# Kernel optimization log

Hardware: AMD Instinct MI355X
Metric: run time of the kernel (lower is better)

## Reference

```python
import jax, jax.numpy as jnp
from jax import lax
import numpy as np

B, C_IN, H, W = 8, 64, 128, 128
C_OUT, K = 64, 3
STRIDE, PAD, DIL = 1, 1, 1
KK = K * K
H_OUT = (H + 2 * PAD - DIL * (K - 1) - 1) // STRIDE + 1
W_OUT = (W + 2 * PAD - DIL * (K - 1) - 1) // STRIDE + 1


def setup_inputs() -> dict:
    key = jax.random.key(0)
    k1, k2, k3, k4 = jax.random.split(key, 4)
    x = jax.random.normal(k1, (B, C_IN, H, W), jnp.float32)
    # offset-predicting conv params (zero-init in the module; use small random
    # values so the deformable sampling path is actually exercised)
    offset_w = jax.random.normal(k2, (2 * KK, C_IN, K, K), jnp.float32) * 0.01
    offset_b = jax.random.normal(k3, (2 * KK,), jnp.float32) * 0.01
    weight = jax.random.normal(k4, (C_OUT, C_IN, K, K), jnp.float32) * (1.0 / np.sqrt(C_IN * KK))
    return {"x": x, "offset_w": offset_w, "offset_b": offset_b, "weight": weight}


def reference(x, offset_w, offset_b, weight):
    # 1) predict offsets: [B, 2*K*K, Hout, Wout], layout (dy, dx) per kernel tap
    offset = lax.conv_general_dilated(
        x, offset_w, (STRIDE, STRIDE), ((PAD, PAD), (PAD, PAD)),
        rhs_dilation=(DIL, DIL), dimension_numbers=("NCHW", "OIHW", "NCHW"))
    offset = offset + offset_b[None, :, None, None]
    off = offset.reshape(B, KK, 2, H_OUT, W_OUT)
    dy = off[:, :, 0].transpose(0, 2, 3, 1)  # [B, Hout, Wout, KK]
    dx = off[:, :, 1].transpose(0, 2, 3, 1)

    # 2) absolute sampling positions p = base_grid + learned offset
    ki, kj = jnp.meshgrid(jnp.arange(K), jnp.arange(K), indexing="ij")
    ki = ki.reshape(-1)
    kj = kj.reshape(-1)
    base_y = (jnp.arange(H_OUT) * STRIDE - PAD)[:, None, None] + ki[None, None, :] * DIL
    base_x = (jnp.arange(W_OUT) * STRIDE - PAD)[None, :, None] + kj[None, None, :] * DIL
    py = base_y[None].astype(x.dtype) + dy  # [B, Hout, Wout, KK]
    px = base_x[None].astype(x.dtype) + dx

    y0 = jnp.floor(py)
    x0 = jnp.floor(px)
    wy1 = py - y0
    wy0 = 1.0 - wy1
    wx1 = px - x0
    wx0 = 1.0 - wx1
    y0i = y0.astype(jnp.int32)
    x0i = x0.astype(jnp.int32)
    y1i = y0i + 1
    x1i = x0i + 1

    L = H_OUT * W_OUT * KK
    f = lambda a: a.reshape(B, L)

    def gather(xb, yi, xi):
        # xb: [C, H, W]; yi, xi: [L] int; zero outside the image
        valid = ((yi >= 0) & (yi < H) & (xi >= 0) & (xi < W)).astype(xb.dtype)
        idx = jnp.clip(yi, 0, H - 1) * W + jnp.clip(xi, 0, W - 1)
        return jnp.take(xb.reshape(C_IN, H * W), idx, axis=1) * valid[None]

    def per_batch(xb, y0i, y1i, x0i, x1i, wy0, wy1, wx0, wx1):
        return (gather(xb, y0i, x0i) * (wy0 * wx0)[None]
                + gather(xb, y0i, x1i) * (wy0 * wx1)[None]
                + gather(xb, y1i, x0i) * (wy1 * wx0)[None]
                + gather(xb, y1i, x1i) * (wy1 * wx1)[None])  # [C, L]

    sampled = jax.vmap(per_batch)(x, f(y0i), f(y1i), f(x0i), f(x1i),
                                  f(wy0), f(wy1), f(wx0), f(wx1))  # [B, C, L]
    sampled = sampled.reshape(B, C_IN, H_OUT, W_OUT, KK)

    # 3) im2col-style contraction against the conv weight (bias=None)
    out = jnp.einsum("bchwk,ock->bohw", sampled, weight.reshape(C_OUT, C_IN, KK))
    return out
```

## Files before the change

### kernel.cpp

```cpp
#include <hip/hip_runtime.h>

#define BATCH 8
#define CIN   64
#define COUT  64
#define HDIM  128
#define WDIM  128
#define HW    (HDIM * WDIM)
#define KK    9

typedef __attribute__((ext_vector_type(8)))  short  short8v;
typedef __attribute__((ext_vector_type(8)))  __bf16 bf16x8;
typedef __attribute__((ext_vector_type(16))) float  f32x16;
typedef float __attribute__((ext_vector_type(2), aligned(4))) float2u;

__device__ __forceinline__ short f2bf(float f) {
    unsigned u = __float_as_uint(f);
    return (short)((u + 0x7fffu + ((u >> 16) & 1u)) >> 16);
}
__device__ __forceinline__ float bf2f(short s) {
    return __uint_as_float(((unsigned)(unsigned short)s) << 16);
}
__device__ __forceinline__ f32x16 mfma_bf16(short8v a, short8v b, f32x16 c) {
    return __builtin_amdgcn_mfma_f32_32x32x16_bf16(
        __builtin_bit_cast(bf16x8, a), __builtin_bit_cast(bf16x8, b), c, 0, 0, 0);
}

__global__ __launch_bounds__(64) void wprep_kernel(
    const float* __restrict__ w, short* __restrict__ Wf)
{
    const int l   = threadIdx.x;
    const int blk = blockIdx.x;
    const int mt  = blk & 1;
    const int s   = blk >> 1;
    const int cg  = s / 9;
    const int t   = s - cg * 9;
    const int oc  = mt * 32 + (l & 31);
    const int cb  = cg * 16 + (l >> 5) * 8;
    short* p0 = Wf + ((size_t)blk * 2 + 0) * 512 + l * 8;
    short* p1 = Wf + ((size_t)blk * 2 + 1) * 512 + l * 8;
#pragma unroll
    for (int e = 0; e < 8; ++e) {
        float v = w[((size_t)oc * CIN + (cb + e)) * KK + t];
        short h = f2bf(v);
        p0[e] = h;
        p1[e] = f2bf(v - bf2f(h));
    }
}

__global__ __launch_bounds__(256) void offset_conv_kernel(
    const float* __restrict__ x,
    const float* __restrict__ ow,
    const float* __restrict__ ob,
    float* __restrict__ py,
    float* __restrict__ px)
{
    __shared__ float Xs[2][4][132];

    const int tid = threadIdx.x;
    const int lin = blockIdx.x;
    const int b   = lin & 7;
    const int par = (lin >> 3) & 1;
    const int pg  = lin >> 4;
    const int h0  = pg * 2;
    const int hh  = tid >> 7;
    const int w   = tid & 127;

    if (tid < 16) {
        const int bu = tid >> 3, r = (tid >> 1) & 3, side = tid & 1;
        Xs[bu][r][1 + side * 129] = 0.0f;
    }

    float acc[9];
#pragma unroll
    for (int i = 0; i < 9; ++i) acc[i] = ob[2 * i + par];

    const float* xb = x + (size_t)b * CIN * HW;

    const int st_r   = tid >> 6;
    const int st_col = (tid * 2) & 127;
    const int st_y   = h0 - 1 + st_r;
    const bool st_v  = (unsigned)st_y < (unsigned)HDIM;
    const float* st_src = xb + (size_t)st_y * WDIM + st_col;

    float2 ld;
    auto issue = [&](int c) {
        ld = st_v ? *(const float2*)(st_src + (size_t)c * HW)
                  : make_float2(0.0f, 0.0f);
    };
    auto write = [&](int bu) {
        *(float2*)&Xs[bu][st_r][2 + st_col] = ld;
    };

    issue(0);
    write(0);
    __syncthreads();

    for (int c = 0; c < CIN; ++c) {
        const int bu = c & 1;
        if (c + 1 < CIN) issue(c + 1);

        float tv[9];
#pragma unroll
        for (int di = 0; di < 3; ++di)
#pragma unroll
            for (int dj = 0; dj < 3; ++dj)
                tv[di * 3 + dj] = Xs[bu][hh + di][w + dj + 1];

        const float* wb = ow + (size_t)par * (CIN * 9) + c * 9;
#pragma unroll
        for (int i = 0; i < 9; ++i) {
            const float* wp = wb + (size_t)i * (2 * CIN * 9);
#pragma unroll
            for (int t = 0; t < 9; ++t) acc[i] = fmaf(tv[t], wp[t], acc[i]);
        }

        if (c + 1 < CIN) write(bu ^ 1);
        __syncthreads();
    }

    const int pixel = pg * 256 + tid;
    float* dst = par ? px : py;
#pragma unroll
    for (int i = 0; i < 9; ++i) {
        const int ki = i / 3, kj = i % 3;
        const float base = par ? (float)(w - 1 + kj) : (float)((h0 + hh) - 1 + ki);
        dst[((size_t)b * KK + i) * HW + pixel] = base + acc[i];
    }
}

__global__ __launch_bounds__(256)
__attribute__((amdgpu_waves_per_eu(2, 4)))
void deform_mfma_kernel(
    const float* __restrict__ x,
    const short* __restrict__ Wf,
    const float* __restrict__ py,
    const float* __restrict__ px_,
    float* __restrict__ out)
{
    __shared__ float Xw[8][16][128];

    const int tid = threadIdx.x;
    const int blk = blockIdx.x;
    const int b  = blk & 7;
    const int h  = blk >> 3;
    const int l  = tid & 63;
    const int wv = tid >> 6;
    const int mypx = 32 * wv + (l & 31);
    const int ch8  = (l >> 5) * 8;

    f32x16 acc0, acc1;
#pragma unroll
    for (int i = 0; i < 16; ++i) { acc0[i] = 0.f; acc1[i] = 0.f; }

    const float* xb = x + (size_t)b * CIN * HW;
    const float* pyb = py  + (size_t)b * KK * HW + h * WDIM + mypx;
    const float* pxb = px_ + (size_t)b * KK * HW + h * WDIM + mypx;

    auto stage = [&](int cg) {
#pragma unroll
        for (int i = 0; i < 16; ++i) {
            const int f = i * 256 + tid;
            const int r   = f >> 9;
            const int c   = (f >> 5) & 15;
            const int col = (f & 31) * 4;
            const int y = h - 3 + r;
            float4 v = make_float4(0.f, 0.f, 0.f, 0.f);
            if ((unsigned)y < (unsigned)HDIM)
                v = *(const float4*)(xb + (size_t)(cg * 16 + c) * HW + y * WDIM + col);
            *(float4*)&Xw[r][c][col] = v;
        }
    };

    float pyc = pyb[0], pxc = pxb[0];

    for (int cg = 0; cg < 4; ++cg) {
        __syncthreads();
        stage(cg);
        __syncthreads();

        for (int t = 0; t < 9; ++t) {
            const int s = cg * 9 + t;

            const short* wf = Wf + (size_t)(s * 4) * 512;
            const short8v w0h = *(const short8v*)(wf + 0 * 512 + l * 8);
            const short8v w0l = *(const short8v*)(wf + 1 * 512 + l * 8);
            const short8v w1h = *(const short8v*)(wf + 2 * 512 + l * 8);
            const short8v w1l = *(const short8v*)(wf + 3 * 512 + l * 8);

            const float y0f = floorf(pyc), x0f = floorf(pxc);
            const float fy = pyc - y0f, fx = pxc - x0f;
            const int y0 = (int)y0f, x0 = (int)x0f;
            const bool vy0 = (unsigned)y0 < (unsigned)HDIM;
            const bool vy1 = (unsigned)(y0 + 1) < (unsigned)HDIM;
            const bool vx0 = (unsigned)x0 < (unsigned)WDIM;
            const bool vx1 = (unsigned)(x0 + 1) < (unsigned)WDIM;
            const int cy0 = min(max(y0, 0), HDIM - 1);
            const int cy1 = min(max(y0 + 1, 0), HDIM - 1);
            const int axc = min(max(x0, 0), WDIM - 2);
            const float wxL = vx0 ? (1.f - fx) : 0.f;
            const float wxR = vx1 ? fx : 0.f;
            float cgx, cgy;
            if (x0 < 0)              { cgx = wxR; cgy = 0.f; }
            else if (x0 >= WDIM - 1) { cgx = 0.f; cgy = wxL; }
            else                     { cgx = wxL; cgy = wxR; }
            const float wy0v = vy0 ? (1.f - fy) : 0.f;
            const float wy1v = vy1 ? fy : 0.f;
            const float a0  = wy0v * cgx, b0c = wy0v * cgy;
            const float a2  = wy1v * cgx, b2c = wy1v * cgy;

            const int t2 = (t + 1) % 9;
            pyc = pyb[(size_t)t2 * HW];
            pxc = pxb[(size_t)t2 * HW];

            const int r0 = cy0 - (h - 3), r1 = cy1 - (h - 3);
            const bool oob = ((unsigned)r0 > 7u) | ((unsigned)r1 > 7u);

            float v[8];
            if (!oob) {
#pragma unroll
                for (int e = 0; e < 8; ++e) {
                    const float2u p0 = *(const float2u*)&Xw[r0][ch8 + e][axc];
                    const float2u p1 = *(const float2u*)&Xw[r1][ch8 + e][axc];
                    float s0 = p0.x * a0;
                    s0 = fmaf(p0.y, b0c, s0);
                    s0 = fmaf(p1.x, a2,  s0);
                    s0 = fmaf(p1.y, b2c, s0);
                    v[e] = s0;
                }
            } else {
                const int cbase = cg * 16 + ch8;
#pragma unroll
                for (int e = 0; e < 8; ++e) {
                    const float* xc = xb + (size_t)(cbase + e) * HW;
                    float s0 = xc[cy0 * WDIM + axc] * a0;
                    s0 = fmaf(xc[cy0 * WDIM + axc + 1], b0c, s0);
                    s0 = fmaf(xc[cy1 * WDIM + axc],     a2,  s0);
                    s0 = fmaf(xc[cy1 * WDIM + axc + 1], b2c, s0);
                    v[e] = s0;
                }
            }

            short8v bh, bl;
#pragma unroll
            for (int e = 0; e < 8; ++e) {
                const short hs = f2bf(v[e]);
                bh[e] = hs;
                bl[e] = f2bf(v[e] - bf2f(hs));
            }

            acc0 = mfma_bf16(w0h, bh, acc0);
            acc1 = mfma_bf16(w1h, bh, acc1);
            acc0 = mfma_bf16(w0l, bh, acc0);
            acc1 = mfma_bf16(w1l, bh, acc1);
            acc0 = mfma_bf16(w0h, bl, acc0);
            acc1 = mfma_bf16(w1h, bl, acc1);
        }
    }

    float* ob = out + (size_t)b * COUT * HW + h * WDIM + 32 * wv + (l & 31);
#pragma unroll
    for (int r = 0; r < 16; ++r) {
        const int oc0 = (r & 3) + 8 * (r >> 2) + 4 * (l >> 5);
        ob[(size_t)oc0 * HW]        = acc0[r];
        ob[(size_t)(oc0 + 32) * HW] = acc1[r];
    }
}

extern "C" void kernel_launch(void* const* d_in, const int* in_sizes, int n_in,
                              void* d_out, int out_size, void* d_ws, size_t ws_size,
                              hipStream_t stream)
{
    const float* x   = (const float*)d_in[0];
    const float* ow  = (const float*)d_in[1];
    const float* obi = (const float*)d_in[2];
    const float* wgt = (const float*)d_in[3];
    float* out = (float*)d_out;

    float* pyw = (float*)d_ws;
    float* pxw = pyw + (size_t)BATCH * KK * HW;
    short* Wf  = (short*)(pxw + (size_t)BATCH * KK * HW);

    wprep_kernel<<<dim3(72), 64, 0, stream>>>(wgt, Wf);
    offset_conv_kernel<<<dim3(1024), 256, 0, stream>>>(x, ow, obi, pyw, pxw);
    deform_mfma_kernel<<<dim3(1024), 256, 0, stream>>>(x, Wf, pyw, pxw, out);
}
```

Baseline: 213.9 us.

## Stage four channels per sync in offset conv; two output rows per deform block

The offset conv now loads and double-buffers four input channels per iteration, so it needs 16 barriers instead of 64 and keeps more loads in flight. The deformable kernel now runs 512 threads per block covering two output rows, and stages a 9-row input window shared by both rows. Each staged row is reused by twice as many pixels and the block count halves. The cost is more shared memory and registers per block, and a block-level occupancy limit of 4 waves per EU that may squeeze registers.

```diff
diff --git a/kernel.cpp b/kernel.cpp
--- a/kernel.cpp
+++ b/kernel.cpp
@@ -54,7 +54,7 @@
     float* __restrict__ py,
     float* __restrict__ px)
 {
-    __shared__ float Xs[2][4][132];
+    __shared__ float Xs[2][4][4][132];
 
     const int tid = threadIdx.x;
     const int lin = blockIdx.x;
@@ -65,9 +65,9 @@
     const int hh  = tid >> 7;
     const int w   = tid & 127;
 
-    if (tid < 16) {
-        const int bu = tid >> 3, r = (tid >> 1) & 3, side = tid & 1;
-        Xs[bu][r][1 + side * 129] = 0.0f;
+    if (tid < 64) {
+        const int bu = tid >> 5, j = (tid >> 3) & 3, r = (tid >> 1) & 3, side = tid & 1;
+        Xs[bu][j][r][1 + side * 129] = 0.0f;
     }
 
     float acc[9];
@@ -82,39 +82,47 @@
     const bool st_v  = (unsigned)st_y < (unsigned)HDIM;
     const float* st_src = xb + (size_t)st_y * WDIM + st_col;
 
-    float2 ld;
-    auto issue = [&](int c) {
-        ld = st_v ? *(const float2*)(st_src + (size_t)c * HW)
-                  : make_float2(0.0f, 0.0f);
+    float2 ld[4];
+    auto issue = [&](int g) {
+#pragma unroll
+        for (int j = 0; j < 4; ++j)
+            ld[j] = st_v ? *(const float2*)(st_src + (size_t)(g * 4 + j) * HW)
+                         : make_float2(0.0f, 0.0f);
     };
     auto write = [&](int bu) {
-        *(float2*)&Xs[bu][st_r][2 + st_col] = ld;
+#pragma unroll
+        for (int j = 0; j < 4; ++j)
+            *(float2*)&Xs[bu][j][st_r][2 + st_col] = ld[j];
     };
 
     issue(0);
     write(0);
     __syncthreads();
 
-    for (int c = 0; c < CIN; ++c) {
-        const int bu = c & 1;
-        if (c + 1 < CIN) issue(c + 1);
-
-        float tv[9];
-#pragma unroll
-        for (int di = 0; di < 3; ++di)
-#pragma unroll
-            for (int dj = 0; dj < 3; ++dj)
-                tv[di * 3 + dj] = Xs[bu][hh + di][w + dj + 1];
-
-        const float* wb = ow + (size_t)par * (CIN * 9) + c * 9;
-#pragma unroll
-        for (int i = 0; i < 9; ++i) {
-            const float* wp = wb + (size_t)i * (2 * CIN * 9);
-#pragma unroll
-            for (int t = 0; t < 9; ++t) acc[i] = fmaf(tv[t], wp[t], acc[i]);
+    for (int g = 0; g < 16; ++g) {
+        const int bu = g & 1;
+        if (g + 1 < 16) issue(g + 1);
+
+#pragma unroll
+        for (int j = 0; j < 4; ++j) {
+            const int c = g * 4 + j;
+            float tv[9];
+#pragma unroll
+            for (int di = 0; di < 3; ++di)
+#pragma unroll
+                for (int dj = 0; dj < 3; ++dj)
+                    tv[di * 3 + dj] = Xs[bu][j][hh + di][w + dj + 1];
+
+            const float* wb = ow + (size_t)par * (CIN * 9) + c * 9;
+#pragma unroll
+            for (int i = 0; i < 9; ++i) {
+                const float* wp = wb + (size_t)i * (2 * CIN * 9);
+#pragma unroll
+                for (int t = 0; t < 9; ++t) acc[i] = fmaf(tv[t], wp[t], acc[i]);
+            }
         }
 
-        if (c + 1 < CIN) write(bu ^ 1);
+        if (g + 1 < 16) write(bu ^ 1);
         __syncthreads();
     }
 
@@ -128,8 +136,8 @@
     }
 }
 
-__global__ __launch_bounds__(256)
-__attribute__((amdgpu_waves_per_eu(2, 4)))
+__global__ __launch_bounds__(512)
+__attribute__((amdgpu_waves_per_eu(4, 4)))
 void deform_mfma_kernel(
     const float* __restrict__ x,
     const short* __restrict__ Wf,
@@ -137,15 +145,16 @@
     const float* __restrict__ px_,
     float* __restrict__ out)
 {
-    __shared__ float Xw[8][16][128];
+    __shared__ float Xw[9][16][128];
 
     const int tid = threadIdx.x;
     const int blk = blockIdx.x;
-    const int b  = blk & 7;
-    const int h  = blk >> 3;
-    const int l  = tid & 63;
-    const int wv = tid >> 6;
-    const int mypx = 32 * wv + (l & 31);
+    const int b   = blk & 7;
+    const int h0  = (blk >> 3) * 2;
+    const int l   = tid & 63;
+    const int wv  = tid >> 6;
+    const int hrow = h0 + (wv >> 2);
+    const int mypx = 32 * (wv & 3) + (l & 31);
     const int ch8  = (l >> 5) * 8;
 
     f32x16 acc0, acc1;
@@ -153,17 +162,17 @@
     for (int i = 0; i < 16; ++i) { acc0[i] = 0.f; acc1[i] = 0.f; }
 
     const float* xb = x + (size_t)b * CIN * HW;
-    const float* pyb = py  + (size_t)b * KK * HW + h * WDIM + mypx;
-    const float* pxb = px_ + (size_t)b * KK * HW + h * WDIM + mypx;
+    const float* pyb = py  + (size_t)b * KK * HW + hrow * WDIM + mypx;
+    const float* pxb = px_ + (size_t)b * KK * HW + hrow * WDIM + mypx;
 
     auto stage = [&](int cg) {
 #pragma unroll
-        for (int i = 0; i < 16; ++i) {
-            const int f = i * 256 + tid;
+        for (int i = 0; i < 9; ++i) {
+            const int f = i * 512 + tid;
             const int r   = f >> 9;
             const int c   = (f >> 5) & 15;
             const int col = (f & 31) * 4;
-            const int y = h - 3 + r;
+            const int y = h0 - 3 + r;
             float4 v = make_float4(0.f, 0.f, 0.f, 0.f);
             if ((unsigned)y < (unsigned)HDIM)
                 v = *(const float4*)(xb + (size_t)(cg * 16 + c) * HW + y * WDIM + col);
@@ -212,8 +221,8 @@
             pyc = pyb[(size_t)t2 * HW];
             pxc = pxb[(size_t)t2 * HW];
 
-            const int r0 = cy0 - (h - 3), r1 = cy1 - (h - 3);
-            const bool oob = ((unsigned)r0 > 7u) | ((unsigned)r1 > 7u);
+            const int r0 = cy0 - (h0 - 3), r1 = cy1 - (h0 - 3);
+            const bool oob = ((unsigned)r0 > 8u) | ((unsigned)r1 > 8u);
 
             float v[8];
             if (!oob) {
@@ -257,7 +266,8 @@
         }
     }
 
-    float* ob = out + (size_t)b * COUT * HW + h * WDIM + 32 * wv + (l & 31);
+    float* ob = out + (size_t)b * COUT * HW + (size_t)hrow * WDIM
+              + 32 * (wv & 3) + (l & 31);
 #pragma unroll
     for (int r = 0; r < 16; ++r) {
         const int oc0 = (r & 3) + 8 * (r >> 2) + 4 * (l >> 5);
@@ -282,5 +292,5 @@
 
     wprep_kernel<<<dim3(72), 64, 0, stream>>>(wgt, Wf);
     offset_conv_kernel<<<dim3(1024), 256, 0, stream>>>(x, ow, obi, pyw, pxw);
-    deform_mfma_kernel<<<dim3(1024), 256, 0, stream>>>(x, Wf, pyw, pxw, out);
-}
+    deform_mfma_kernel<<<dim3(512), 512, 0, stream>>>(x, Wf, pyw, pxw, out);
+}
```

Measured after the change: 250.3 us. 17.0% more time.

## Compute offset-prediction conv with bf16 MFMA instead of scalar FP32 FMAs

Applied to the files above, without the earlier changes.

Rewrites the offset-predicting convolution as an implicit GEMM on 32x32x16 bf16 MFMA instructions. A new prep kernel packs the 18 offset filters, zero-padded to 32 rows, into MFMA-ready bf16 fragments. Each block stages one output row plus halo for 16 input channels at a time in LDS and converts the activations to bf16 before each MFMA. This is meant to cut the ALU cost of the scalar FP32 FMA loop. In exchange it wastes 14 of the 32 MFMA rows and uses single bf16 precision for the offsets, with no hi/lo split, which could perturb the sampling positions.

```diff
diff --git a/kernel.cpp b/kernel.cpp
--- a/kernel.cpp
+++ b/kernel.cpp
@@ -47,84 +47,98 @@
     }
 }
 
+__global__ __launch_bounds__(64) void wprep_off_kernel(
+    const float* __restrict__ ow, short* __restrict__ Wo)
+{
+    const int l  = threadIdx.x;
+    const int s  = blockIdx.x;
+    const int cg = s / 9;
+    const int t  = s - cg * 9;
+    const int oc = l & 31;
+    const int cb = cg * 16 + (l >> 5) * 8;
+    short* p = Wo + (size_t)s * 512 + l * 8;
+#pragma unroll
+    for (int e = 0; e < 8; ++e) {
+        float v = (oc < 18) ? ow[((size_t)oc * CIN + (cb + e)) * KK + t] : 0.0f;
+        p[e] = f2bf(v);
+    }
+}
+
 __global__ __launch_bounds__(256) void offset_conv_kernel(
     const float* __restrict__ x,
-    const float* __restrict__ ow,
+    const short* __restrict__ Wo,
     const float* __restrict__ ob,
     float* __restrict__ py,
     float* __restrict__ px)
 {
-    __shared__ float Xs[2][4][132];
+    __shared__ float Xo[3][16][136];
 
     const int tid = threadIdx.x;
-    const int lin = blockIdx.x;
-    const int b   = lin & 7;
-    const int par = (lin >> 3) & 1;
-    const int pg  = lin >> 4;
-    const int h0  = pg * 2;
-    const int hh  = tid >> 7;
-    const int w   = tid & 127;
-
-    if (tid < 16) {
-        const int bu = tid >> 3, r = (tid >> 1) & 3, side = tid & 1;
-        Xs[bu][r][1 + side * 129] = 0.0f;
-    }
-
-    float acc[9];
-#pragma unroll
-    for (int i = 0; i < 9; ++i) acc[i] = ob[2 * i + par];
+    const int blk = blockIdx.x;
+    const int b   = blk & 7;
+    const int h   = blk >> 3;
+    const int l   = tid & 63;
+    const int wv  = tid >> 6;
+    const int pcol = 32 * wv + (l & 31);
+    const int ch8  = (l >> 5) * 8;
+
+    f32x16 acc;
+#pragma unroll
+    for (int i = 0; i < 16; ++i) acc[i] = 0.f;
 
     const float* xb = x + (size_t)b * CIN * HW;
 
-    const int st_r   = tid >> 6;
-    const int st_col = (tid * 2) & 127;
-    const int st_y   = h0 - 1 + st_r;
-    const bool st_v  = (unsigned)st_y < (unsigned)HDIM;
-    const float* st_src = xb + (size_t)st_y * WDIM + st_col;
-
-    float2 ld;
-    auto issue = [&](int c) {
-        ld = st_v ? *(const float2*)(st_src + (size_t)c * HW)
-                  : make_float2(0.0f, 0.0f);
+    if (tid < 96) {
+        const int r = tid >> 5, cc = (tid >> 1) & 15, side = tid & 1;
+        Xo[r][cc][3 + side * 129] = 0.0f;
+    }
+
+    auto stage = [&](int cg) {
+#pragma unroll
+        for (int i = 0; i < 6; ++i) {
+            const int f = i * 256 + tid;
+            const int r   = f >> 9;
+            const int cc  = (f >> 5) & 15;
+            const int col = (f & 31) * 4;
+            const int y = h - 1 + r;
+            float4 v = make_float4(0.f, 0.f, 0.f, 0.f);
+            if ((unsigned)y < (unsigned)HDIM)
+                v = *(const float4*)(xb + (size_t)(cg * 16 + cc) * HW + y * WDIM + col);
+            *(float4*)&Xo[r][cc][4 + col] = v;
+        }
     };
-    auto write = [&](int bu) {
-        *(float2*)&Xs[bu][st_r][2 + st_col] = ld;
-    };
-
-    issue(0);
-    write(0);
-    __syncthreads();
-
-    for (int c = 0; c < CIN; ++c) {
-        const int bu = c & 1;
-        if (c + 1 < CIN) issue(c + 1);
-
-        float tv[9];
-#pragma unroll
-        for (int di = 0; di < 3; ++di)
-#pragma unroll
-            for (int dj = 0; dj < 3; ++dj)
-                tv[di * 3 + dj] = Xs[bu][hh + di][w + dj + 1];
-
-        const float* wb = ow + (size_t)par * (CIN * 9) + c * 9;
-#pragma unroll
-        for (int i = 0; i < 9; ++i) {
-            const float* wp = wb + (size_t)i * (2 * CIN * 9);
-#pragma unroll
-            for (int t = 0; t < 9; ++t) acc[i] = fmaf(tv[t], wp[t], acc[i]);
-        }
-
-        if (c + 1 < CIN) write(bu ^ 1);
+
+    for (int cg = 0; cg < 4; ++cg) {
         __syncthreads();
-    }
-
-    const int pixel = pg * 256 + tid;
-    float* dst = par ? px : py;
-#pragma unroll
-    for (int i = 0; i < 9; ++i) {
-        const int ki = i / 3, kj = i % 3;
-        const float base = par ? (float)(w - 1 + kj) : (float)((h0 + hh) - 1 + ki);
-        dst[((size_t)b * KK + i) * HW + pixel] = base + acc[i];
+        stage(cg);
+        __syncthreads();
+
+#pragma unroll
+        for (int t = 0; t < 9; ++t) {
+            const int s = cg * 9 + t;
+            const short8v wo = *(const short8v*)(Wo + (size_t)s * 512 + l * 8);
+
+            const int ki = t / 3, kj = t % 3;
+            short8v bh;
+#pragma unroll
+            for (int e = 0; e < 8; ++e)
+                bh[e] = f2bf(Xo[ki][ch8 + e][3 + pcol + kj]);
+
+            acc = mfma_bf16(wo, bh, acc);
+        }
+    }
+
+#pragma unroll
+    for (int r = 0; r < 16; ++r) {
+        const int oc0 = (r & 3) + 8 * (r >> 2) + 4 * (l >> 5);
+        if (oc0 < 18) {
+            const int kk = oc0 >> 1, par = oc0 & 1;
+            const float base = par ? (float)(pcol - 1 + (kk % 3))
+                                   : (float)(h - 1 + (kk / 3));
+            float* dst = (par ? px : py)
+                       + ((size_t)b * KK + kk) * HW + h * WDIM + pcol;
+            *dst = base + acc[r] + ob[oc0];
+        }
     }
 }
 
@@ -279,8 +293,10 @@
     float* pyw = (float*)d_ws;
     float* pxw = pyw + (size_t)BATCH * KK * HW;
     short* Wf  = (short*)(pxw + (size_t)BATCH * KK * HW);
+    short* Wo  = Wf + (size_t)72 * 2 * 512;
 
     wprep_kernel<<<dim3(72), 64, 0, stream>>>(wgt, Wf);
-    offset_conv_kernel<<<dim3(1024), 256, 0, stream>>>(x, ow, obi, pyw, pxw);
+    wprep_off_kernel<<<dim3(36), 64, 0, stream>>>(ow, Wo);
+    offset_conv_kernel<<<dim3(1024), 256, 0, stream>>>(x, Wo, obi, pyw, pxw);
     deform_mfma_kernel<<<dim3(1024), 256, 0, stream>>>(x, Wf, pyw, pxw, out);
 }
```

After: 183.1 us. 1.17x faster.
